# Kernel optimization log

Measured on AMD Instinct MI355X. Metric: run time of the kernel, lower is better.

Reference implementation:

```python
import jax, jax.numpy as jnp
import numpy as np

N_NODES = 16384   # n_nodes
N_LINKS = 8192    # batch of target links
D_EMB = 128       # embedding dim
EDGE_P = 0.004    # adjacency density -> avg degree ~65


def setup_inputs() -> dict:
    key = jax.random.key(0)
    k1, k2, k3 = jax.random.split(key, 3)
    adj = jax.random.bernoulli(k1, EDGE_P, (N_NODES, N_NODES))
    adj = adj | adj.T                      # symmetric graph
    adj = adj & ~jnp.eye(N_NODES, dtype=bool)  # no self loops
    links = jax.random.randint(k2, (N_LINKS, 2), 0, N_NODES)
    emb = jax.random.normal(k3, (N_NODES, D_EMB), dtype=jnp.float32)
    return {"targetLink": links, "adjacent": adj, "NodeEmbedding": emb}


def reference(targetLink, adjacent, NodeEmbedding):
    # targetLink: [B,2] int, adjacent: [N,N] bool, NodeEmbedding: [N,D] float
    i = targetLink[:, 0]
    j = targetLink[:, 1]
    emb_i = NodeEmbedding[i]               # [B,D] gather
    emb_j = NodeEmbedding[j]               # [B,D] gather
    product = emb_i * emb_j                # [B,D]
    # common-neighbor indicator: u is a CN of (i,j) iff adj[i,u] and adj[j,u]
    cn_mask = (adjacent[i] & adjacent[j]).astype(NodeEmbedding.dtype)  # [B,N]
    # sum of embeddings over common neighbors (fused gather-reduce)
    cn_sum = cn_mask @ NodeEmbedding       # [B,D]
    return jnp.concatenate([product, cn_sum], axis=-1)  # [B,2D]
```

## Files before the change

kernel.cpp:

```cpp
#include <hip/hip_runtime.h>

#define N_NODES 16384
#define D_EMB   128
#define LIST_CAP 1024
#define BM_U64   256
#define FLAG_OFF N_NODES
#define CNT_OFF  (N_NODES + 1)
#define LIST_OFF (N_NODES + 8)
#define BM_OFF_BYTES (1 << 18)
#define WS_NEEDED (BM_OFF_BYTES + (size_t)N_NODES * (BM_U64 * 8))

__global__ __launch_bounds__(256) void zero_probe_kernel(
    const unsigned int* __restrict__ words, int* __restrict__ flags)
{
    if (blockIdx.x < 64) {
        flags[blockIdx.x * 256 + threadIdx.x] = 0;
    } else {
        __shared__ int s_any;
        if (threadIdx.x == 0) { s_any = 0; flags[CNT_OFF] = 0; }
        __syncthreads();
        int any = 0;
        for (int k = threadIdx.x; k < 16384; k += 256)
            if (words[k] > 1u) any = 1;
        if (any) atomicOr(&s_any, 1);
        __syncthreads();
        if (threadIdx.x == 0) flags[FLAG_OFF] = s_any;
    }
}

__global__ __launch_bounds__(256) void mark_list_kernel(
    const int* __restrict__ links, int* __restrict__ flags, int n_endpoints)
{
    const int e = blockIdx.x * 256 + threadIdx.x;
    if (e >= n_endpoints) return;
    const int r = links[e];
    if (atomicCAS(&flags[r], 0, 1) == 0) {
        const int pos = atomicAdd(&flags[CNT_OFF], 1);
        flags[LIST_OFF + pos] = r;
    }
}

__global__ __launch_bounds__(256) void compress_pair_kernel(
    const void* __restrict__ adjv, const int* __restrict__ flags,
    unsigned long long* __restrict__ bm64)
{
    const int n_used = flags[CNT_OFF];
    const int i0 = 2 * blockIdx.x;
    const int i1 = i0 + 1;
    if (i0 >= n_used) return;
    const int r0 = flags[LIST_OFF + i0];
    const int r1 = (i1 < n_used) ? flags[LIST_OFF + i1] : -1;
    const int t = threadIdx.x;
    const int byte_layout = flags[FLAG_OFF];

    if (!byte_layout) {
        const uint4* rowA = reinterpret_cast<const uint4*>(
            (const int*)adjv + (size_t)r0 * N_NODES);
        if (r1 >= 0) {
            const uint4* rowB = reinterpret_cast<const uint4*>(
                (const int*)adjv + (size_t)r1 * N_NODES);
            unsigned int lo0 = 0u, hi0 = 0u, lo1 = 0u, hi1 = 0u;
#pragma unroll
            for (int k = 0; k < 8; ++k) {
                const uint4 a = rowA[k * 256 + t];
                const uint4 b = rowB[k * 256 + t];
                lo0 |= (min(a.x,1u) | (min(a.y,1u)<<1) | (min(a.z,1u)<<2) | (min(a.w,1u)<<3)) << (4*k);
                lo1 |= (min(b.x,1u) | (min(b.y,1u)<<1) | (min(b.z,1u)<<2) | (min(b.w,1u)<<3)) << (4*k);
            }
#pragma unroll
            for (int k = 8; k < 16; ++k) {
                const uint4 a = rowA[k * 256 + t];
                const uint4 b = rowB[k * 256 + t];
                hi0 |= (min(a.x,1u) | (min(a.y,1u)<<1) | (min(a.z,1u)<<2) | (min(a.w,1u)<<3)) << (4*(k-8));
                hi1 |= (min(b.x,1u) | (min(b.y,1u)<<1) | (min(b.z,1u)<<2) | (min(b.w,1u)<<3)) << (4*(k-8));
            }
            bm64[(size_t)r0 * BM_U64 + t] = ((unsigned long long)hi0 << 32) | lo0;
            bm64[(size_t)r1 * BM_U64 + t] = ((unsigned long long)hi1 << 32) | lo1;
        } else {
            unsigned int lo0 = 0u, hi0 = 0u;
#pragma unroll
            for (int k = 0; k < 8; ++k) {
                const uint4 a = rowA[k * 256 + t];
                lo0 |= (min(a.x,1u) | (min(a.y,1u)<<1) | (min(a.z,1u)<<2) | (min(a.w,1u)<<3)) << (4*k);
            }
#pragma unroll
            for (int k = 8; k < 16; ++k) {
                const uint4 a = rowA[k * 256 + t];
                hi0 |= (min(a.x,1u) | (min(a.y,1u)<<1) | (min(a.z,1u)<<2) | (min(a.w,1u)<<3)) << (4*(k-8));
            }
            bm64[(size_t)r0 * BM_U64 + t] = ((unsigned long long)hi0 << 32) | lo0;
        }
    } else {
        for (int s = 0; s < 2; ++s) {
            const int r = (s == 0) ? r0 : r1;
            if (r < 0) break;
            const uint4* row = reinterpret_cast<const uint4*>(
                (const unsigned char*)adjv + (size_t)r * N_NODES);
            unsigned long long bits = 0ull;
#pragma unroll
            for (int q = 0; q < 4; ++q) {
                const uint4 v = row[t * 4 + q];
                const unsigned int arr[4] = {v.x, v.y, v.z, v.w};
#pragma unroll
                for (int a = 0; a < 4; ++a)
#pragma unroll
                    for (int bb = 0; bb < 4; ++bb)
                        if ((arr[a] >> (8 * bb)) & 0xFFu)
                            bits |= 1ull << (q * 16 + a * 4 + bb);
            }
            bm64[(size_t)r * BM_U64 + t] = bits;
        }
    }
}

__global__ __launch_bounds__(256) void link_kernel(
    const int* __restrict__ links, const unsigned long long* __restrict__ bm64,
    const float* __restrict__ emb, float* __restrict__ out,
    const int* __restrict__ flags, int n_links)
{
    const int link = blockIdx.x;
    if (link >= n_links) return;
    const int i = links[2 * link];
    const int j = links[2 * link + 1];
    const int byte_layout = flags[FLAG_OFF];

    __shared__ int s_list[LIST_CAP];
    __shared__ int s_count;
    if (threadIdx.x == 0) s_count = 0;
    __syncthreads();

    const int t = threadIdx.x;
    unsigned long long m = bm64[(size_t)i * BM_U64 + t]
                         & bm64[(size_t)j * BM_U64 + t];
    while (m) {
        const int b = __ffsll(m) - 1;
        m &= m - 1;
        const int node = byte_layout
            ? (t * 64 + b)
            : (((b >> 2) << 10) + (t << 2) + (b & 3));
        const int pos = atomicAdd(&s_count, 1);
        if (pos < LIST_CAP) s_list[pos] = node;
    }
    __syncthreads();

    int count = s_count;
    if (count > LIST_CAP) count = LIST_CAP;

    const size_t obase = (size_t)link * (2 * D_EMB);
    if (t < D_EMB) {
        out[obase + t] = emb[(size_t)i * D_EMB + t] * emb[(size_t)j * D_EMB + t];
    } else {
        const int d = t - D_EMB;
        float s = 0.0f;
        for (int c = 0; c < count; ++c)
            s += emb[(size_t)s_list[c] * D_EMB + d];
        out[obase + D_EMB + d] = s;
    }
}

__global__ __launch_bounds__(256) void detect_layout_kernel(
    const unsigned int* __restrict__ words, int* __restrict__ flag)
{
    __shared__ int s_any;
    if (threadIdx.x == 0) s_any = 0;
    __syncthreads();
    int any = 0;
    for (int k = threadIdx.x; k < 16384; k += 256)
        if (words[k] > 1u) any = 1;
    if (any) atomicOr(&s_any, 1);
    __syncthreads();
    if (threadIdx.x == 0) *flag = s_any;
}

__global__ __launch_bounds__(256) void ncn_direct(
    const int* __restrict__ links, const void* __restrict__ adjv,
    const float* __restrict__ emb, float* __restrict__ out,
    const int* __restrict__ flag, int n_links)
{
    const int link = blockIdx.x;
    if (link >= n_links) return;
    const int i = links[2 * link];
    const int j = links[2 * link + 1];

    __shared__ int s_list[LIST_CAP];
    __shared__ int s_count;
    if (threadIdx.x == 0) s_count = 0;
    __syncthreads();

    const int byte_layout = flag ? flag[0] : 0;
    if (byte_layout) {
        const uint4* rowi = reinterpret_cast<const uint4*>(
            (const unsigned char*)adjv + (size_t)i * N_NODES);
        const uint4* rowj = reinterpret_cast<const uint4*>(
            (const unsigned char*)adjv + (size_t)j * N_NODES);
#pragma unroll
        for (int c = 0; c < 4; ++c) {
            const int idx = c * 256 + threadIdx.x;
            const uint4 a = rowi[idx];
            const uint4 bq = rowj[idx];
            unsigned int m[4] = {a.x & bq.x, a.y & bq.y, a.z & bq.z, a.w & bq.w};
            if (m[0] | m[1] | m[2] | m[3]) {
                const int base = idx * 16;
#pragma unroll
                for (int w = 0; w < 4; ++w) {
                    unsigned int v = m[w];
                    if (!v) continue;
#pragma unroll
                    for (int b8 = 0; b8 < 4; ++b8) {
                        if ((v >> (8 * b8)) & 0xFFu) {
                            int pos = atomicAdd(&s_count, 1);
                            if (pos < LIST_CAP) s_list[pos] = base + w * 4 + b8;
                        }
                    }
                }
            }
        }
    } else {
        const uint4* rowi = reinterpret_cast<const uint4*>(
            (const int*)adjv + (size_t)i * N_NODES);
        const uint4* rowj = reinterpret_cast<const uint4*>(
            (const int*)adjv + (size_t)j * N_NODES);
#pragma unroll
        for (int c = 0; c < 16; ++c) {
            const int idx = c * 256 + threadIdx.x;
            const uint4 a = rowi[idx];
            const uint4 bq = rowj[idx];
            const int base = idx * 4;
            if (a.x & bq.x) { int p = atomicAdd(&s_count, 1); if (p < LIST_CAP) s_list[p] = base + 0; }
            if (a.y & bq.y) { int p = atomicAdd(&s_count, 1); if (p < LIST_CAP) s_list[p] = base + 1; }
            if (a.z & bq.z) { int p = atomicAdd(&s_count, 1); if (p < LIST_CAP) s_list[p] = base + 2; }
            if (a.w & bq.w) { int p = atomicAdd(&s_count, 1); if (p < LIST_CAP) s_list[p] = base + 3; }
        }
    }
    __syncthreads();

    int count = s_count;
    if (count > LIST_CAP) count = LIST_CAP;

    const int t = threadIdx.x;
    const size_t obase = (size_t)link * (2 * D_EMB);
    if (t < D_EMB) {
        out[obase + t] = emb[(size_t)i * D_EMB + t] * emb[(size_t)j * D_EMB + t];
    } else {
        const int d = t - D_EMB;
        float s = 0.0f;
        for (int c = 0; c < count; ++c)
            s += emb[(size_t)s_list[c] * D_EMB + d];
        out[obase + D_EMB + d] = s;
    }
}

extern "C" void kernel_launch(void* const* d_in, const int* in_sizes, int n_in,
                              void* d_out, int out_size, void* d_ws, size_t ws_size,
                              hipStream_t stream) {
    const int* links = (const int*)d_in[0];
    const void* adj = d_in[1];
    const float* emb = (const float*)d_in[2];
    float* out = (float*)d_out;

    const int n_links = in_sizes[0] / 2;

    if (ws_size >= WS_NEEDED) {
        int* flags = (int*)d_ws;
        unsigned long long* bm64 =
            (unsigned long long*)((char*)d_ws + BM_OFF_BYTES);

        zero_probe_kernel<<<65, 256, 0, stream>>>(
            (const unsigned int*)adj, flags);
        mark_list_kernel<<<(2 * n_links + 255) / 256, 256, 0, stream>>>(
            links, flags, 2 * n_links);
        compress_pair_kernel<<<N_NODES / 2, 256, 0, stream>>>(
            adj, flags, bm64);
        link_kernel<<<n_links, 256, 0, stream>>>(
            links, bm64, emb, out, flags, n_links);
    } else {
        int* flag = (ws_size >= sizeof(int)) ? (int*)d_ws : nullptr;
        if (flag) detect_layout_kernel<<<1, 256, 0, stream>>>(
            (const unsigned int*)adj, flag);
        ncn_direct<<<n_links, 256, 0, stream>>>(links, adj, emb, out, flag, n_links);
    }
}
```

Measured before the change: 181.3 us.

## Split row compression into quarter-row tasks with 64-thread blocks and new bit layout

```diff
diff --git a/kernel.cpp b/kernel.cpp
--- a/kernel.cpp
+++ b/kernel.cpp
@@ -9,6 +9,7 @@
 #define LIST_OFF (N_NODES + 8)
 #define BM_OFF_BYTES (1 << 18)
 #define WS_NEEDED (BM_OFF_BYTES + (size_t)N_NODES * (BM_U64 * 8))
+#define CGRID 16384
 
 __global__ __launch_bounds__(256) void zero_probe_kernel(
     const unsigned int* __restrict__ words, int* __restrict__ flags)
@@ -40,75 +41,57 @@
     }
 }
 
-__global__ __launch_bounds__(256) void compress_pair_kernel(
+__global__ __launch_bounds__(64) void compress_tasks_kernel(
     const void* __restrict__ adjv, const int* __restrict__ flags,
     unsigned long long* __restrict__ bm64)
 {
     const int n_used = flags[CNT_OFF];
-    const int i0 = 2 * blockIdx.x;
-    const int i1 = i0 + 1;
-    if (i0 >= n_used) return;
-    const int r0 = flags[LIST_OFF + i0];
-    const int r1 = (i1 < n_used) ? flags[LIST_OFF + i1] : -1;
+    const int n_tasks = 4 * n_used;
     const int t = threadIdx.x;
     const int byte_layout = flags[FLAG_OFF];
 
-    if (!byte_layout) {
-        const uint4* rowA = reinterpret_cast<const uint4*>(
-            (const int*)adjv + (size_t)r0 * N_NODES);
-        if (r1 >= 0) {
-            const uint4* rowB = reinterpret_cast<const uint4*>(
-                (const int*)adjv + (size_t)r1 * N_NODES);
-            unsigned int lo0 = 0u, hi0 = 0u, lo1 = 0u, hi1 = 0u;
-#pragma unroll
-            for (int k = 0; k < 8; ++k) {
-                const uint4 a = rowA[k * 256 + t];
-                const uint4 b = rowB[k * 256 + t];
-                lo0 |= (min(a.x,1u) | (min(a.y,1u)<<1) | (min(a.z,1u)<<2) | (min(a.w,1u)<<3)) << (4*k);
-                lo1 |= (min(b.x,1u) | (min(b.y,1u)<<1) | (min(b.z,1u)<<2) | (min(b.w,1u)<<3)) << (4*k);
-            }
-#pragma unroll
-            for (int k = 8; k < 16; ++k) {
-                const uint4 a = rowA[k * 256 + t];
-                const uint4 b = rowB[k * 256 + t];
-                hi0 |= (min(a.x,1u) | (min(a.y,1u)<<1) | (min(a.z,1u)<<2) | (min(a.w,1u)<<3)) << (4*(k-8));
-                hi1 |= (min(b.x,1u) | (min(b.y,1u)<<1) | (min(b.z,1u)<<2) | (min(b.w,1u)<<3)) << (4*(k-8));
-            }
-            bm64[(size_t)r0 * BM_U64 + t] = ((unsigned long long)hi0 << 32) | lo0;
-            bm64[(size_t)r1 * BM_U64 + t] = ((unsigned long long)hi1 << 32) | lo1;
+    for (int task = blockIdx.x; task < n_tasks; task += CGRID) {
+        const int r = flags[LIST_OFF + (task >> 2)];
+        const int Q = task & 3;
+
+        if (!byte_layout) {
+            const uint4* qrow = reinterpret_cast<const uint4*>(
+                (const int*)adjv + (size_t)r * N_NODES) + Q * 1024;
+            unsigned int lo = 0u, hi = 0u;
+#pragma unroll
+            for (int q = 0; q < 8; ++q) {
+                const uint4 v = qrow[q * 64 + t];
+                const unsigned int nib = min(v.x,1u) | (min(v.y,1u)<<1)
+                                       | (min(v.z,1u)<<2) | (min(v.w,1u)<<3);
+                lo |= nib << (4 * q);
+            }
+#pragma unroll
+            for (int q = 8; q < 16; ++q) {
+                const uint4 v = qrow[q * 64 + t];
+                const unsigned int nib = min(v.x,1u) | (min(v.y,1u)<<1)
+                                       | (min(v.z,1u)<<2) | (min(v.w,1u)<<3);
+                hi |= nib << (4 * (q - 8));
+            }
+            bm64[(size_t)r * BM_U64 + Q * 64 + t] =
+                ((unsigned long long)hi << 32) | lo;
         } else {
-            unsigned int lo0 = 0u, hi0 = 0u;
-#pragma unroll
-            for (int k = 0; k < 8; ++k) {
-                const uint4 a = rowA[k * 256 + t];
-                lo0 |= (min(a.x,1u) | (min(a.y,1u)<<1) | (min(a.z,1u)<<2) | (min(a.w,1u)<<3)) << (4*k);
-            }
-#pragma unroll
-            for (int k = 8; k < 16; ++k) {
-                const uint4 a = rowA[k * 256 + t];
-                hi0 |= (min(a.x,1u) | (min(a.y,1u)<<1) | (min(a.z,1u)<<2) | (min(a.w,1u)<<3)) << (4*(k-8));
-            }
-            bm64[(size_t)r0 * BM_U64 + t] = ((unsigned long long)hi0 << 32) | lo0;
-        }
-    } else {
-        for (int s = 0; s < 2; ++s) {
-            const int r = (s == 0) ? r0 : r1;
-            if (r < 0) break;
-            const uint4* row = reinterpret_cast<const uint4*>(
-                (const unsigned char*)adjv + (size_t)r * N_NODES);
+            const uint4* qrow = reinterpret_cast<const uint4*>(
+                (const unsigned char*)adjv + (size_t)r * N_NODES) + Q * 256;
             unsigned long long bits = 0ull;
 #pragma unroll
             for (int q = 0; q < 4; ++q) {
-                const uint4 v = row[t * 4 + q];
+                const uint4 v = qrow[q * 64 + t];
                 const unsigned int arr[4] = {v.x, v.y, v.z, v.w};
+                unsigned int half = 0;
 #pragma unroll
                 for (int a = 0; a < 4; ++a)
 #pragma unroll
                     for (int bb = 0; bb < 4; ++bb)
-                        if ((arr[a] >> (8 * bb)) & 0xFFu)
-                            bits |= 1ull << (q * 16 + a * 4 + bb);
-            }
-            bm64[(size_t)r * BM_U64 + t] = bits;
+                        half |= ((((arr[a] >> (8 * bb)) & 0xFFu) ? 1u : 0u)
+                                 << (a * 4 + bb));
+                bits |= (unsigned long long)half << (16 * q);
+            }
+            bm64[(size_t)r * BM_U64 + Q * 64 + t] = bits;
         }
     }
 }
@@ -136,8 +119,8 @@
         const int b = __ffsll(m) - 1;
         m &= m - 1;
         const int node = byte_layout
-            ? (t * 64 + b)
-            : (((b >> 2) << 10) + (t << 2) + (b & 3));
+            ? (((t >> 6) << 12) + ((b >> 4) << 10) + ((t & 63) << 4) + (b & 15))
+            : (((t >> 6) << 12) + ((b >> 2) << 8) + ((t & 63) << 2) + (b & 3));
         const int pos = atomicAdd(&s_count, 1);
         if (pos < LIST_CAP) s_list[pos] = node;
     }
@@ -269,7 +252,7 @@
             (const unsigned int*)adj, flags);
         mark_list_kernel<<<(2 * n_links + 255) / 256, 256, 0, stream>>>(
             links, flags, 2 * n_links);
-        compress_pair_kernel<<<N_NODES / 2, 256, 0, stream>>>(
+        compress_tasks_kernel<<<CGRID, 64, 0, stream>>>(
             adj, flags, bm64);
         link_kernel<<<n_links, 256, 0, stream>>>(
             links, bm64, emb, out, flags, n_links);
```

Result: no change. 177.8 us (-1.9%).
